# Kernel tuning notes

Hardware: AMD Instinct MI355X
Metric: run time of the kernel (lower is better)

Reference implementation:

```python
import jax, jax.numpy as jnp
import numpy as np

B, Z_DIM, T_DIM, ACT_E, CF, N_ACT, STEPS = 256, 256, 512, 256, 1024, 64, 64


def setup_inputs() -> dict:
    key = jax.random.key(0)
    ks = jax.random.split(key, 12)
    s = 0.02
    def n(k, shape):
        return jax.random.normal(k, shape, jnp.float32) * s
    return {
        "z": jax.random.normal(ks[0], (B, Z_DIM), jnp.float32),
        "W_z2t": n(ks[1], (T_DIM, Z_DIM)), "b_z2t": jnp.zeros((T_DIM,), jnp.float32),
        "E": n(ks[2], (N_ACT, ACT_E)),  # encoder_act2e embedding table
        "Wih_a": n(ks[3], (4 * CF, T_DIM + ACT_E)), "Whh_a": n(ks[4], (4 * CF, CF)),
        "bih_a": jnp.zeros((4 * CF,), jnp.float32), "bhh_a": jnp.zeros((4 * CF,), jnp.float32),
        "Wih_t": n(ks[5], (4 * CF, T_DIM + ACT_E + 1)), "Whh_t": n(ks[6], (4 * CF, CF)),
        "bih_t": jnp.zeros((4 * CF,), jnp.float32), "bhh_t": jnp.zeros((4 * CF,), jnp.float32),
        "W_act": n(ks[7], (N_ACT, CF)), "b_act": jnp.zeros((N_ACT,), jnp.float32),
        "W_ts1": n(ks[8], (CF // 2, CF)), "b_ts1": jnp.zeros((CF // 2,), jnp.float32),
        "W_ts2": n(ks[9], (1, CF // 2)), "b_ts2": jnp.zeros((1,), jnp.float32),
    }


def _lstm_step(x, h, c, Wih, Whh, bih, bhh):
    # PyTorch LSTM gate order: i, f, g, o
    gates = x @ Wih.T + h @ Whh.T + bih + bhh
    i, f, g, o = jnp.split(gates, 4, axis=-1)
    c = jax.nn.sigmoid(f) * c + jax.nn.sigmoid(i) * jnp.tanh(g)
    h = jax.nn.sigmoid(o) * jnp.tanh(c)
    return h, c


def reference(z, W_z2t, b_z2t, E, Wih_a, Whh_a, bih_a, bhh_a,
              Wih_t, Whh_t, bih_t, bhh_t, W_act, b_act,
              W_ts1, b_ts1, W_ts2, b_ts2):
    Bz = z.shape[0]
    t_rec = jax.nn.relu(z @ W_z2t.T + b_z2t)                 # [B, t_dim]
    zeros_h = jnp.zeros((Bz, CF), z.dtype)
    act_emb0 = jnp.broadcast_to(E[-1], (Bz, ACT_E))          # EOT token embedding
    ts0 = jnp.zeros((Bz, 1), z.dtype)

    def step(carry, _):
        h_a, c_a, h_t, c_t, act_emb, ts = carry
        x_a = jnp.concatenate([t_rec, act_emb], axis=1)       # [B, t_dim+act_e]
        h_a, c_a = _lstm_step(x_a, h_a, c_a, Wih_a, Whh_a, bih_a, bhh_a)
        logits = h_a @ W_act.T + b_act                        # [B, num_activities]
        act_emb = E[jnp.argmax(logits, axis=1)]               # [B, act_e]
        x_t = jnp.concatenate([t_rec, act_emb, ts], axis=1)   # [B, t_dim+act_e+1]
        h_t, c_t = _lstm_step(x_t, h_t, c_t, Wih_t, Whh_t, bih_t, bhh_t)
        ts = jax.nn.relu(h_t @ W_ts1.T + b_ts1) @ W_ts2.T + b_ts2  # [B, 1]
        return (h_a, c_a, h_t, c_t, act_emb, ts), (logits, ts)

    carry0 = (zeros_h, zeros_h, zeros_h, zeros_h, act_emb0, ts0)
    _, (logits_seq, ts_seq) = jax.lax.scan(step, carry0, None, length=STEPS)
    acts_rec = jax.nn.softmax(jnp.transpose(logits_seq, (1, 0, 2)), axis=2)  # [B, T, A]
    ts_rec = jnp.transpose(ts_seq[..., 0], (1, 0))                            # [B, T]
    return acts_rec, ts_rec
```

## Files before the change

kernel.cpp:

```cpp
#include <hip/hip_runtime.h>
#include <stdint.h>

typedef unsigned int u32;
typedef float  f32x4 __attribute__((ext_vector_type(4)));
typedef float  f32x2 __attribute__((ext_vector_type(2)));
typedef double f64x2 __attribute__((ext_vector_type(2)));
typedef double f64x4 __attribute__((ext_vector_type(4)));

constexpr int NT = 256;
constexpr int BB = 256;
constexpr int ZD = 256;
constexpr int TD = 512;
constexpr int CF = 1024;
constexpr int G4 = 4096;
constexpr int NA = 64;
constexpr int NSTEP = 64;
constexpr int TS_OFF = BB * NSTEP * NA;

constexpr int RSF = 34;
constexpr int FRS = 68;
constexpr int SMEMB = 2 * 64 * RSF * 8;

struct P {
  const float *z, *W_z2t, *b_z2t, *E, *Wih_a, *Whh_a, *bih_a, *bhh_a,
              *Wih_t, *Whh_t, *bih_t, *bhh_t, *W_act, *b_act, *W_ts1, *b_ts1, *W_ts2, *b_ts2;
  float* out;
  double *t_rec64, *pre_a64, *E_proj_a64, *h_a64, *c_a64, *gacc_a;
  float *t_rec32, *pre_t, *E_proj_t, *colt, *h_t, *c_t, *gacc_t, *ts_accum;
  int* idxb;
};

__device__ __forceinline__ float sigf(float x){ return 1.f / (1.f + expf(-x)); }
__device__ __forceinline__ float tanhf_(float x){
  float ax = fabsf(x); float e = expf(-2.f * ax);
  float t = 1.f - 2.f * e / (1.f + e);
  return x < 0.f ? -t : t;
}
__device__ __forceinline__ double sigd(double x){ return 1.0 / (1.0 + exp(-x)); }

__global__ void __launch_bounds__(NT) k_setup(P p){
  __shared__ double sz[ZD];
  const int bid = blockIdx.x, tid = threadIdx.x;
  for (int i = tid; i < ZD; i += NT) sz[i] = (double)p.z[bid * ZD + i];
  __syncthreads();
  for (int k = tid; k < TD; k += NT){
    const float* wr = p.W_z2t + (size_t)k * ZD;
    double a = 0.0;
    for (int j = 0; j < ZD; ++j) a = fma((double)wr[j], sz[j], a);
    a += (double)p.b_z2t[k];
    double t = a > 0.0 ? a : 0.0;
    p.t_rec64[(size_t)bid * TD + k] = t;
    p.t_rec32[(size_t)bid * TD + k] = (float)t;
  }
  for (int i = tid; i < CF; i += NT){
    p.c_a64[(size_t)bid * CF + i] = 0.0;
    p.h_a64[(size_t)bid * CF + i] = 0.0;
    p.c_t[(size_t)bid * CF + i] = 0.f;
    p.h_t[(size_t)bid * CF + i] = 0.f;
  }
  if (tid == 0){ p.idxb[bid] = NA - 1; p.ts_accum[bid] = 0.f; }
}

__global__ void __launch_bounds__(NT) k_eproj(P p){
  __shared__ double sz[ZD];
  const int bid = blockIdx.x, tid = threadIdx.x;
  if (bid < 256){
    const int erow = bid >> 2, cchunk = bid & 3;
    for (int i = tid; i < ZD; i += NT) sz[i] = (double)p.E[erow * ZD + i];
    __syncthreads();
    for (int ci = 0; ci < 4; ++ci){
      const int c = cchunk * 1024 + ci * 256 + tid;
      const float* wr = p.Wih_a + (size_t)c * 768 + 512;
      double a = 0.0;
      for (int j = 0; j < 256; ++j) a = fma((double)wr[j], sz[j], a);
      p.E_proj_a64[(size_t)erow * G4 + c] = a;
    }
  } else if (bid < 512){
    const int erow = (bid - 256) >> 2, cchunk = (bid - 256) & 3;
    for (int i = tid; i < ZD; i += NT) sz[i] = (double)p.E[erow * ZD + i];
    __syncthreads();
    for (int ci = 0; ci < 4; ++ci){
      const int c = cchunk * 1024 + ci * 256 + tid;
      const float* wr = p.Wih_t + (size_t)c * 769 + 512;
      float a = 0.f;
      for (int j = 0; j < 256; ++j) a = fmaf(wr[j], (float)sz[j], a);
      p.E_proj_t[(size_t)erow * G4 + c] = a;
    }
  } else {
    const int c = (bid - 512) * 256 + tid;
    p.colt[c] = p.Wih_t[(size_t)c * 769 + 768];
  }
}

template <bool A64, bool OUT64, bool BIAS>
__device__ void mgemm64(char* smem, const void* __restrict__ Av, int lda,
                        const float* __restrict__ B, int ldb,
                        int rowb, int colb, int K,
                        const void* __restrict__ addin,
                        const float* __restrict__ bih, const float* __restrict__ bhh,
                        void* __restrict__ outv){
  double* As = (double*)smem;
  double* Bs = As + 64 * RSF;
  const int tid = threadIdx.x;
  const int lane = tid & 63;
  const int wm = (tid >> 7) & 1, wn = (tid >> 6) & 1;
  const int m = lane & 15, q = lane >> 4;
  const int tr = tid >> 2, tkq = tid & 3;
  const double* A64p = (const double*)Av;
  const float*  A32p = (const float*)Av;

  double av[8], bv[8];
  auto loadchunk = [&](int kb){
    if (A64){
      const double* ap = A64p + (size_t)(rowb + tr) * lda + kb + tkq * 8;
      #pragma unroll
      for (int j = 0; j < 8; ++j) av[j] = ap[j];
    } else {
      const float* ap = A32p + (size_t)(rowb + tr) * lda + kb + tkq * 8;
      #pragma unroll
      for (int j = 0; j < 8; ++j) av[j] = (double)ap[j];
    }
    const float* bp = B + (size_t)(colb + tr) * ldb + kb + tkq * 8;
    #pragma unroll
    for (int j = 0; j < 8; ++j) bv[j] = (double)bp[j];
  };
  f64x4 acc[2][2];
  #pragma unroll
  for (int g = 0; g < 2; ++g)
    #pragma unroll
    for (int h = 0; h < 2; ++h) acc[g][h] = f64x4{0.0,0.0,0.0,0.0};

  loadchunk(0);
  for (int kb = 0; kb < K; kb += 32){
    __syncthreads();
    {
      double* arow = As + tr * RSF + tkq * 8;
      double* brow = Bs + tr * RSF + tkq * 8;
      #pragma unroll
      for (int j = 0; j < 4; ++j){
        *(f64x2*)(arow + j * 2) = f64x2{av[j], av[j + 4]};
        *(f64x2*)(brow + j * 2) = f64x2{bv[j], bv[j + 4]};
      }
    }
    __syncthreads();
    if (kb + 32 < K) loadchunk(kb + 32);
    #pragma unroll
    for (int sp = 0; sp < 4; ++sp){
      const f64x2 a0 = *(const f64x2*)(As + (wm * 32 +  0 + m) * RSF + sp * 8 + q * 2);
      const f64x2 a1 = *(const f64x2*)(As + (wm * 32 + 16 + m) * RSF + sp * 8 + q * 2);
      const f64x2 b0 = *(const f64x2*)(Bs + (wn * 32 +  0 + m) * RSF + sp * 8 + q * 2);
      const f64x2 b1 = *(const f64x2*)(Bs + (wn * 32 + 16 + m) * RSF + sp * 8 + q * 2);
      acc[0][0] = __builtin_amdgcn_mfma_f64_16x16x4f64(a0[0], b0[0], acc[0][0], 0, 0, 0);
      acc[0][1] = __builtin_amdgcn_mfma_f64_16x16x4f64(a0[0], b1[0], acc[0][1], 0, 0, 0);
      acc[1][0] = __builtin_amdgcn_mfma_f64_16x16x4f64(a1[0], b0[0], acc[1][0], 0, 0, 0);
      acc[1][1] = __builtin_amdgcn_mfma_f64_16x16x4f64(a1[0], b1[0], acc[1][1], 0, 0, 0);
      acc[0][0] = __builtin_amdgcn_mfma_f64_16x16x4f64(a0[1], b0[1], acc[0][0], 0, 0, 0);
      acc[0][1] = __builtin_amdgcn_mfma_f64_16x16x4f64(a0[1], b1[1], acc[0][1], 0, 0, 0);
      acc[1][0] = __builtin_amdgcn_mfma_f64_16x16x4f64(a1[1], b0[1], acc[1][0], 0, 0, 0);
      acc[1][1] = __builtin_amdgcn_mfma_f64_16x16x4f64(a1[1], b1[1], acc[1][1], 0, 0, 0);
    }
  }
  #pragma unroll
  for (int g = 0; g < 2; ++g){
    const int rb = rowb + wm * 32 + g * 16 + q;
    #pragma unroll
    for (int h = 0; h < 2; ++h){
      const int cc = colb + wn * 32 + h * 16 + m;
      if (BIAS){
        const double bb = (double)bih[cc] + (double)bhh[cc];
        #pragma unroll
        for (int v = 0; v < 4; ++v){
          if (OUT64) ((double*)outv)[(size_t)(rb + 4 * v) * G4 + cc] = acc[g][h][v] + bb;
          else       ((float*) outv)[(size_t)(rb + 4 * v) * G4 + cc] = (float)(acc[g][h][v] + bb);
        }
      } else {
        #pragma unroll
        for (int v = 0; v < 4; ++v){
          const size_t o = (size_t)(rb + 4 * v) * G4 + cc;
          if (OUT64) ((double*)outv)[o] = acc[g][h][v] + ((const double*)addin)[o];
          else       ((float*) outv)[o] = (float)(acc[g][h][v] + (double)((const float*)addin)[o]);
        }
      }
    }
  }
}

template <bool BIAS>
__device__ void dgemm32(char* smem, const float* __restrict__ A, int lda,
                        const float* __restrict__ B, int ldb,
                        int rowb, int colb, int K,
                        const float* __restrict__ addin,
                        const float* __restrict__ bih, const float* __restrict__ bhh,
                        float* __restrict__ outp){
  float* As = (float*)smem;
  float* Bs = (float*)(smem + 64 * FRS * 4);
  const int tid = threadIdx.x;
  const int tx = tid & 15, ty = tid >> 4;
  const int r_ = tid >> 2, kq = tid & 3;
  const int wsw = r_ ^ (kq * 8);
  float acc[4][4];
  #pragma unroll
  for (int i = 0; i < 4; ++i)
    #pragma unroll
    for (int j = 0; j < 4; ++j) acc[i][j] = 0.f;

  float pa[16], pb[16];
  auto ldA = [&](int kb){
    const float* ap = A + (size_t)(rowb + r_) * lda + kb + kq * 16;
    #pragma unroll
    for (int j = 0; j < 16; ++j) pa[j] = ap[j];
  };
  auto ldB = [&](int kb){
    const float* bp = B + (size_t)(colb + r_) * ldb + kb + kq * 16;
    #pragma unroll
    for (int j = 0; j < 16; ++j) pb[j] = bp[j];
  };
  ldA(0); ldB(0);
  for (int kb = 0; kb < K; kb += 64){
    __syncthreads();
    #pragma unroll
    for (int j = 0; j < 16; ++j){
      As[(kq * 16 + j) * FRS + wsw] = pa[j];
      Bs[(kq * 16 + j) * FRS + wsw] = pb[j];
    }
    __syncthreads();
    if (kb + 64 < K){ ldA(kb + 64); ldB(kb + 64); }
    #pragma unroll 4
    for (int k = 0; k < 64; ++k){
      const int sw = (k >> 4) * 8;
      f32x4 a4 = *(const f32x4*)(As + k * FRS + ((4 * ty) ^ sw));
      f32x4 b4 = *(const f32x4*)(Bs + k * FRS + ((4 * tx) ^ sw));
      acc[0][0] = fmaf(a4[0], b4[0], acc[0][0]); acc[0][1] = fmaf(a4[0], b4[1], acc[0][1]);
      acc[0][2] = fmaf(a4[0], b4[2], acc[0][2]); acc[0][3] = fmaf(a4[0], b4[3], acc[0][3]);
      acc[1][0] = fmaf(a4[1], b4[0], acc[1][0]); acc[1][1] = fmaf(a4[1], b4[1], acc[1][1]);
      acc[1][2] = fmaf(a4[1], b4[2], acc[1][2]); acc[1][3] = fmaf(a4[1], b4[3], acc[1][3]);
      acc[2][0] = fmaf(a4[2], b4[0], acc[2][0]); acc[2][1] = fmaf(a4[2], b4[1], acc[2][1]);
      acc[2][2] = fmaf(a4[2], b4[2], acc[2][2]); acc[2][3] = fmaf(a4[2], b4[3], acc[2][3]);
      acc[3][0] = fmaf(a4[3], b4[0], acc[3][0]); acc[3][1] = fmaf(a4[3], b4[1], acc[3][1]);
      acc[3][2] = fmaf(a4[3], b4[2], acc[3][2]); acc[3][3] = fmaf(a4[3], b4[3], acc[3][3]);
    }
  }
  const int c0 = colb + 4 * tx;
  if (BIAS){
    float bb0 = bih[c0+0] + bhh[c0+0], bb1 = bih[c0+1] + bhh[c0+1];
    float bb2 = bih[c0+2] + bhh[c0+2], bb3 = bih[c0+3] + bhh[c0+3];
    #pragma unroll
    for (int i = 0; i < 4; ++i){
      float* o = outp + (size_t)(rowb + 4 * ty + i) * G4 + c0;
      o[0] = acc[i][0] + bb0; o[1] = acc[i][1] + bb1;
      o[2] = acc[i][2] + bb2; o[3] = acc[i][3] + bb3;
    }
  } else {
    #pragma unroll
    for (int i = 0; i < 4; ++i){
      const size_t base = (size_t)(rowb + 4 * ty + i) * G4 + c0;
      const float* ai = addin + base;
      float* o = outp + base;
      o[0] = acc[i][0] + ai[0]; o[1] = acc[i][1] + ai[1];
      o[2] = acc[i][2] + ai[2]; o[3] = acc[i][3] + ai[3];
    }
  }
}

__device__ void tshead_j(const P& p, int bid, int hbuf){
  const int tid = threadIdx.x;
  const int tm = bid >> 6, tjq = bid & 63;
  const int rowb = tm * 32;
  const int rt = tid >> 3, j8 = tid & 7;
  const int j = tjq * 8 + j8;
  const float* __restrict__ hr = p.h_t + (size_t)hbuf * BB * CF + (size_t)(rowb + rt) * CF;
  const float* __restrict__ wr = p.W_ts1 + (size_t)j * CF;
  float a0=0,a1=0,a2=0,a3=0;
  for (int k = 0; k < CF; k += 16){
    f32x4 h0 = *(const f32x4*)(hr + k),     h1 = *(const f32x4*)(hr + k + 4);
    f32x4 h2 = *(const f32x4*)(hr + k + 8), h3 = *(const f32x4*)(hr + k + 12);
    f32x4 w0 = *(const f32x4*)(wr + k),     w1 = *(const f32x4*)(wr + k + 4);
    f32x4 w2 = *(const f32x4*)(wr + k + 8), w3 = *(const f32x4*)(wr + k + 12);
    a0 = fmaf(h0[0],w0[0], fmaf(h0[1],w0[1], fmaf(h0[2],w0[2], fmaf(h0[3],w0[3], a0))));
    a1 = fmaf(h1[0],w1[0], fmaf(h1[1],w1[1], fmaf(h1[2],w1[2], fmaf(h1[3],w1[3], a1))));
    a2 = fmaf(h2[0],w2[0], fmaf(h2[1],w2[1], fmaf(h2[2],w2[2], fmaf(h2[3],w2[3], a2))));
    a3 = fmaf(h3[0],w3[0], fmaf(h3[1],w3[1], fmaf(h3[2],w3[2], fmaf(h3[3],w3[3], a3))));
  }
  float v = ((a0 + a1) + (a2 + a3)) + p.b_ts1[j];
  v = (v > 0.f ? v : 0.f) * p.W_ts2[j];
  v += __shfl_xor(v, 1, 64);
  v += __shfl_xor(v, 2, 64);
  v += __shfl_xor(v, 4, 64);
  if (j8 == 0) atomicAdd(p.ts_accum + rowb + rt, v);
}

__global__ void __launch_bounds__(NT) k_pre(P p){
  __shared__ __align__(16) char smem[SMEMB];
  const int bid = blockIdx.x;
  const int hsel = bid >> 8, sub = bid & 255;
  const int rowb = (sub >> 6) * 64, colb = (sub & 63) * 64;
  if (hsel == 0)
    mgemm64<true, true, true>(smem, p.t_rec64, TD, p.Wih_a, 768, rowb, colb, TD,
                              nullptr, p.bih_a, p.bhh_a, p.pre_a64);
  else
    dgemm32<true>(smem, p.t_rec32, TD, p.Wih_t, 769, rowb, colb, TD,
                  nullptr, p.bih_t, p.bhh_t, p.pre_t);
}

__global__ void __launch_bounds__(NT) k_stepA(P p, int s){
  __shared__ __align__(16) char smem[SMEMB];
  const int bid = blockIdx.x;
  if (s > 0) tshead_j(p, bid, s & 1);
  const int hsel = bid >> 8, sub = bid & 255;
  const int rowb = (sub >> 6) * 64, colb = (sub & 63) * 64;
  const int rd = s & 1;
  if (hsel == 0)
    mgemm64<true, true, false>(smem, p.h_a64 + (size_t)rd * BB * CF, CF, p.Whh_a, CF,
                               rowb, colb, CF, p.pre_a64, nullptr, nullptr, p.gacc_a);
  else
    dgemm32<false>(smem, p.h_t + (size_t)rd * BB * CF, CF, p.Whh_t, CF,
                   rowb, colb, CF, p.pre_t, nullptr, nullptr, p.gacc_t);
}

__global__ void __launch_bounds__(NT) k_stepB(P p, int s){
  __shared__ double shd[1092];
  const int b = blockIdx.x, tid = threadIdx.x;
  const int cur = (s + 1) & 1;
  int idxp = p.idxb[b];
  idxp = idxp < 0 ? 0 : (idxp > 63 ? 63 : idxp);
  {
    const double* ga = p.gacc_a + (size_t)b * G4;
    const double* ea = p.E_proj_a64 + (size_t)idxp * G4;
    const int c0 = tid * 4;
    #pragma unroll
    for (int jj = 0; jj < 4; ++jj){
      const int c = c0 + jj;
      double gi = ga[0*CF + c] + ea[0*CF + c];
      double gf = ga[1*CF + c] + ea[1*CF + c];
      double gg = ga[2*CF + c] + ea[2*CF + c];
      double go = ga[3*CF + c] + ea[3*CF + c];
      double cv = p.c_a64[(size_t)b * CF + c];
      double cn = sigd(gf) * cv + sigd(gi) * tanh(gg);
      double hn = sigd(go) * tanh(cn);
      p.c_a64[(size_t)b * CF + c] = cn;
      p.h_a64[(size_t)cur * BB * CF + (size_t)b * CF + c] = hn;
      shd[c] = hn;
    }
  }
  if (tid == 0) shd[1088] = (s == 0) ? 0.0 : ((double)p.ts_accum[b] + (double)p.b_ts2[0]);
  __syncthreads();
  {
    const int w = tid >> 6, l = tid & 63, l15 = l & 15, quad = l >> 4;
    const int a = w * 16 + l15;
    const float* wr = p.W_act + (size_t)a * CF + quad * 256;
    const double* hp = shd + quad * 256;
    double acc = 0.0;
    for (int kk = 0; kk < 256; kk += 4){
      acc = fma((double)wr[kk+0], hp[kk+0], acc);
      acc = fma((double)wr[kk+1], hp[kk+1], acc);
      acc = fma((double)wr[kk+2], hp[kk+2], acc);
      acc = fma((double)wr[kk+3], hp[kk+3], acc);
    }
    acc += __shfl_xor(acc, 16, 64);
    acc += __shfl_xor(acc, 32, 64);
    if (quad == 0) shd[1024 + a] = acc;
  }
  __syncthreads();
  if (tid < 64){
    double acc = shd[1024 + tid] + (double)p.b_act[tid];
    double m = acc;
    #pragma unroll
    for (int off = 32; off; off >>= 1) m = fmax(m, __shfl_xor(m, off, 64));
    unsigned long long ball = __ballot(acc == m);
    int idxv = __ffsll(ball) - 1;
    idxv = idxv < 0 ? 0 : (idxv > 63 ? 63 : idxv);
    double e = exp(acc - m);
    double ssum = e;
    #pragma unroll
    for (int off = 32; off; off >>= 1) ssum += __shfl_xor(ssum, off, 64);
    p.out[(size_t)b * (NSTEP * NA) + s * NA + tid] = (float)(e / ssum);
    if (tid == 0){
      p.idxb[b] = idxv;
      shd[1089] = (double)idxv;
      if (s > 0) p.out[TS_OFF + b * NSTEP + (s - 1)] = (float)shd[1088];
    }
  }
  __syncthreads();
  const float ts_val = (float)shd[1088];
  const int idxv = (int)shd[1089];
  const int c0 = tid * 4;
  const float* gb = p.gacc_t   + (size_t)b * G4;
  const float* eb = p.E_proj_t + (size_t)idxv * G4;
  f32x4 gi = *(const f32x4*)(gb + 0*CF + c0) + *(const f32x4*)(eb + 0*CF + c0) + ts_val * *(const f32x4*)(p.colt + 0*CF + c0);
  f32x4 gf = *(const f32x4*)(gb + 1*CF + c0) + *(const f32x4*)(eb + 1*CF + c0) + ts_val * *(const f32x4*)(p.colt + 1*CF + c0);
  f32x4 gg = *(const f32x4*)(gb + 2*CF + c0) + *(const f32x4*)(eb + 2*CF + c0) + ts_val * *(const f32x4*)(p.colt + 2*CF + c0);
  f32x4 go = *(const f32x4*)(gb + 3*CF + c0) + *(const f32x4*)(eb + 3*CF + c0) + ts_val * *(const f32x4*)(p.colt + 3*CF + c0);
  f32x4 cv = *(f32x4*)(p.c_t + (size_t)b * CF + c0);
  f32x4 cn, hn;
  #pragma unroll
  for (int jj = 0; jj < 4; ++jj){
    float cj = sigf(gf[jj]) * cv[jj] + sigf(gi[jj]) * tanhf_(gg[jj]);
    float hj = sigf(go[jj]) * tanhf_(cj);
    cn[jj] = cj; hn[jj] = hj;
  }
  *(f32x4*)(p.c_t + (size_t)b * CF + c0) = cn;
  *(f32x4*)(p.h_t + (size_t)cur * BB * CF + (size_t)b * CF + c0) = hn;
  __syncthreads();
  if (tid == 0) p.ts_accum[b] = 0.f;
}

__global__ void __launch_bounds__(NT) k_tsfin(P p){
  tshead_j(p, blockIdx.x, 0);
}
__global__ void __launch_bounds__(NT) k_tswrite(P p){
  p.out[TS_OFF + threadIdx.x * NSTEP + 63] = p.ts_accum[threadIdx.x] + p.b_ts2[0];
}

extern "C" void kernel_launch(void* const* d_in, const int* in_sizes, int n_in,
                              void* d_out, int out_size, void* d_ws, size_t ws_size,
                              hipStream_t stream){
  (void)in_sizes; (void)n_in; (void)out_size; (void)ws_size;
  P p;
  p.z     = (const float*)d_in[0];  p.W_z2t = (const float*)d_in[1];  p.b_z2t = (const float*)d_in[2];
  p.E     = (const float*)d_in[3];  p.Wih_a = (const float*)d_in[4];  p.Whh_a = (const float*)d_in[5];
  p.bih_a = (const float*)d_in[6];  p.bhh_a = (const float*)d_in[7];  p.Wih_t = (const float*)d_in[8];
  p.Whh_t = (const float*)d_in[9];  p.bih_t = (const float*)d_in[10]; p.bhh_t = (const float*)d_in[11];
  p.W_act = (const float*)d_in[12]; p.b_act = (const float*)d_in[13]; p.W_ts1 = (const float*)d_in[14];
  p.b_ts1 = (const float*)d_in[15]; p.W_ts2 = (const float*)d_in[16]; p.b_ts2 = (const float*)d_in[17];
  p.out = (float*)d_out;
  char* w = (char*)d_ws;
  size_t off = 0;
  auto alloc = [&](size_t bytes) -> void* { void* r = w + off; off += (bytes + 255) & ~(size_t)255; return r; };
  p.t_rec64    = (double*)alloc((size_t)BB * TD * 8);
  p.pre_a64    = (double*)alloc((size_t)BB * G4 * 8);
  p.E_proj_a64 = (double*)alloc((size_t)NA * G4 * 8);
  p.h_a64      = (double*)alloc((size_t)2 * BB * CF * 8);
  p.c_a64      = (double*)alloc((size_t)BB * CF * 8);
  p.gacc_a     = (double*)alloc((size_t)BB * G4 * 8);
  p.t_rec32    = (float*)alloc((size_t)BB * TD * 4);
  p.pre_t      = (float*)alloc((size_t)BB * G4 * 4);
  p.E_proj_t   = (float*)alloc((size_t)NA * G4 * 4);
  p.colt       = (float*)alloc((size_t)G4 * 4);
  p.h_t        = (float*)alloc((size_t)2 * BB * CF * 4);
  p.c_t        = (float*)alloc((size_t)BB * CF * 4);
  p.gacc_t     = (float*)alloc((size_t)BB * G4 * 4);
  p.ts_accum   = (float*)alloc((size_t)BB * 4);
  p.idxb       = (int*)  alloc((size_t)BB * 4);

  k_setup<<<dim3(256), dim3(NT), 0, stream>>>(p);
  k_eproj<<<dim3(528), dim3(NT), 0, stream>>>(p);
  k_pre  <<<dim3(512), dim3(NT), 0, stream>>>(p);
  for (int s = 0; s < NSTEP; ++s){
    k_stepA<<<dim3(512), dim3(NT), 0, stream>>>(p, s);
    k_stepB<<<dim3(256), dim3(NT), 0, stream>>>(p, s);
  }
  k_tsfin  <<<dim3(512), dim3(NT), 0, stream>>>(p);
  k_tswrite<<<dim3(1),   dim3(NT), 0, stream>>>(p);
}
```

Measured before the change: 11.42 ms.

## Replace LDS-staged recurrent GEMMs with direct global-load register-pipelined GEMMs

The per-step recurrent GEMMs (h_a@Whh_a in fp64 MFMA and h_t@Whh_t in fp32 FMA) now load operands straight from global memory into registers with a two-stage software prefetch, instead of staging tiles through shared memory with __syncthreads. The goal is to remove LDS traffic, barriers and shared-memory occupancy limits from the step kernel. The trade-off is that the new loads are strided and uncoalesced per lane and operands are fetched redundantly across threads, so the kernel depends on L1/L2 cache hits. The prologue GEMM keeps the old LDS path, now specialized to bias-only.

```diff
diff --git a/kernel.cpp b/kernel.cpp
--- a/kernel.cpp
+++ b/kernel.cpp
@@ -20,6 +20,7 @@
 constexpr int RSF = 34;
 constexpr int FRS = 68;
 constexpr int SMEMB = 2 * 64 * RSF * 8;
+
 
 struct P {
   const float *z, *W_z2t, *b_z2t, *E, *Wih_a, *Whh_a, *bih_a, *bhh_a,
@@ -92,11 +93,10 @@
   }
 }
 
-template <bool A64, bool OUT64, bool BIAS>
+template <bool A64, bool OUT64>
 __device__ void mgemm64(char* smem, const void* __restrict__ Av, int lda,
                         const float* __restrict__ B, int ldb,
                         int rowb, int colb, int K,
-                        const void* __restrict__ addin,
                         const float* __restrict__ bih, const float* __restrict__ bhh,
                         void* __restrict__ outv){
   double* As = (double*)smem;
@@ -166,30 +166,19 @@
     #pragma unroll
     for (int h = 0; h < 2; ++h){
       const int cc = colb + wn * 32 + h * 16 + m;
-      if (BIAS){
-        const double bb = (double)bih[cc] + (double)bhh[cc];
-        #pragma unroll
-        for (int v = 0; v < 4; ++v){
-          if (OUT64) ((double*)outv)[(size_t)(rb + 4 * v) * G4 + cc] = acc[g][h][v] + bb;
-          else       ((float*) outv)[(size_t)(rb + 4 * v) * G4 + cc] = (float)(acc[g][h][v] + bb);
-        }
-      } else {
-        #pragma unroll
-        for (int v = 0; v < 4; ++v){
-          const size_t o = (size_t)(rb + 4 * v) * G4 + cc;
-          if (OUT64) ((double*)outv)[o] = acc[g][h][v] + ((const double*)addin)[o];
-          else       ((float*) outv)[o] = (float)(acc[g][h][v] + (double)((const float*)addin)[o]);
-        }
+      const double bb = (double)bih[cc] + (double)bhh[cc];
+      #pragma unroll
+      for (int v = 0; v < 4; ++v){
+        if (OUT64) ((double*)outv)[(size_t)(rb + 4 * v) * G4 + cc] = acc[g][h][v] + bb;
+        else       ((float*) outv)[(size_t)(rb + 4 * v) * G4 + cc] = (float)(acc[g][h][v] + bb);
       }
     }
   }
 }
 
-template <bool BIAS>
 __device__ void dgemm32(char* smem, const float* __restrict__ A, int lda,
                         const float* __restrict__ B, int ldb,
                         int rowb, int colb, int K,
-                        const float* __restrict__ addin,
                         const float* __restrict__ bih, const float* __restrict__ bhh,
                         float* __restrict__ outp){
   float* As = (float*)smem;
@@ -241,24 +230,129 @@
     }
   }
   const int c0 = colb + 4 * tx;
-  if (BIAS){
-    float bb0 = bih[c0+0] + bhh[c0+0], bb1 = bih[c0+1] + bhh[c0+1];
-    float bb2 = bih[c0+2] + bhh[c0+2], bb3 = bih[c0+3] + bhh[c0+3];
-    #pragma unroll
-    for (int i = 0; i < 4; ++i){
-      float* o = outp + (size_t)(rowb + 4 * ty + i) * G4 + c0;
-      o[0] = acc[i][0] + bb0; o[1] = acc[i][1] + bb1;
-      o[2] = acc[i][2] + bb2; o[3] = acc[i][3] + bb3;
-    }
-  } else {
-    #pragma unroll
-    for (int i = 0; i < 4; ++i){
-      const size_t base = (size_t)(rowb + 4 * ty + i) * G4 + c0;
-      const float* ai = addin + base;
-      float* o = outp + base;
-      o[0] = acc[i][0] + ai[0]; o[1] = acc[i][1] + ai[1];
-      o[2] = acc[i][2] + ai[2]; o[3] = acc[i][3] + ai[3];
-    }
+  float bb0 = bih[c0+0] + bhh[c0+0], bb1 = bih[c0+1] + bhh[c0+1];
+  float bb2 = bih[c0+2] + bhh[c0+2], bb3 = bih[c0+3] + bhh[c0+3];
+  #pragma unroll
+  for (int i = 0; i < 4; ++i){
+    float* o = outp + (size_t)(rowb + 4 * ty + i) * G4 + c0;
+    o[0] = acc[i][0] + bb0; o[1] = acc[i][1] + bb1;
+    o[2] = acc[i][2] + bb2; o[3] = acc[i][3] + bb3;
+  }
+}
+
+template <bool A64, bool OUT64>
+__device__ void mgemm64d(const void* __restrict__ Av, int lda,
+                         const float* __restrict__ B, int ldb,
+                         int rowb, int colb, int K,
+                         const void* __restrict__ addin, void* __restrict__ outv){
+  const int tid = threadIdx.x, lane = tid & 63;
+  const int wm = (tid >> 7) & 1, wn = (tid >> 6) & 1;
+  const int m = lane & 15, q = lane >> 4;
+  const double* Ar0 = (const double*)Av + (size_t)(rowb + wm * 32 +  0 + m) * lda;
+  const double* Ar1 = (const double*)Av + (size_t)(rowb + wm * 32 + 16 + m) * lda;
+  const float*  Af0 = (const float*) Av + (size_t)(rowb + wm * 32 +  0 + m) * lda;
+  const float*  Af1 = (const float*) Av + (size_t)(rowb + wm * 32 + 16 + m) * lda;
+  const float*  Bc0 = B + (size_t)(colb + wn * 32 +  0 + m) * ldb;
+  const float*  Bc1 = B + (size_t)(colb + wn * 32 + 16 + m) * ldb;
+  f64x4 c00{0,0,0,0}, c01{0,0,0,0}, c10{0,0,0,0}, c11{0,0,0,0};
+  double xA00,xA04,xA10,xA14,xB00,xB04,xB10,xB14;
+  double yA00,yA04,yA10,yA14,yB00,yB04,yB10,yB14;
+#define ALD(S, g) do{ const int _k = 8 * (g) + q;                                 \
+    S##A00 = A64 ? Ar0[_k]     : (double)Af0[_k];                                 \
+    S##A04 = A64 ? Ar0[_k + 4] : (double)Af0[_k + 4];                             \
+    S##A10 = A64 ? Ar1[_k]     : (double)Af1[_k];                                 \
+    S##A14 = A64 ? Ar1[_k + 4] : (double)Af1[_k + 4];                             \
+    S##B00 = (double)Bc0[_k];   S##B04 = (double)Bc0[_k + 4];                     \
+    S##B10 = (double)Bc1[_k];   S##B14 = (double)Bc1[_k + 4]; }while(0)
+#define AMF(S) do{                                                                \
+    c00 = __builtin_amdgcn_mfma_f64_16x16x4f64(S##A00, S##B00, c00, 0, 0, 0);     \
+    c01 = __builtin_amdgcn_mfma_f64_16x16x4f64(S##A00, S##B10, c01, 0, 0, 0);     \
+    c10 = __builtin_amdgcn_mfma_f64_16x16x4f64(S##A10, S##B00, c10, 0, 0, 0);     \
+    c11 = __builtin_amdgcn_mfma_f64_16x16x4f64(S##A10, S##B10, c11, 0, 0, 0);     \
+    c00 = __builtin_amdgcn_mfma_f64_16x16x4f64(S##A04, S##B04, c00, 0, 0, 0);     \
+    c01 = __builtin_amdgcn_mfma_f64_16x16x4f64(S##A04, S##B14, c01, 0, 0, 0);     \
+    c10 = __builtin_amdgcn_mfma_f64_16x16x4f64(S##A14, S##B04, c10, 0, 0, 0);     \
+    c11 = __builtin_amdgcn_mfma_f64_16x16x4f64(S##A14, S##B14, c11, 0, 0, 0); }while(0)
+  const int NG = K >> 3;
+  ALD(x, 0);
+  for (int g = 0; g < NG; g += 2){
+    ALD(y, g + 1);
+    AMF(x);
+    if (g + 2 < NG) ALD(x, g + 2);
+    AMF(y);
+  }
+#undef ALD
+#undef AMF
+  #pragma unroll
+  for (int g = 0; g < 2; ++g){
+    const int rb = rowb + wm * 32 + g * 16 + q;
+    #pragma unroll
+    for (int h = 0; h < 2; ++h){
+      const f64x4 a = g ? (h ? c11 : c10) : (h ? c01 : c00);
+      const int cc = colb + wn * 32 + h * 16 + m;
+      #pragma unroll
+      for (int v = 0; v < 4; ++v){
+        const size_t o = (size_t)(rb + 4 * v) * G4 + cc;
+        if (OUT64) ((double*)outv)[o] = a[v] + ((const double*)addin)[o];
+        else       ((float*) outv)[o] = (float)(a[v] + (double)((const float*)addin)[o]);
+      }
+    }
+  }
+}
+
+__device__ void dgemm32d(const float* __restrict__ A, int lda,
+                         const float* __restrict__ B, int ldb,
+                         int rowb, int colb, int K,
+                         const float* __restrict__ addin, float* __restrict__ outp){
+  const int tid = threadIdx.x;
+  const int tx = tid & 15, ty = tid >> 4;
+  const float* ar0 = A + (size_t)(rowb + 4 * ty + 0) * lda;
+  const float* ar1 = A + (size_t)(rowb + 4 * ty + 1) * lda;
+  const float* ar2 = A + (size_t)(rowb + 4 * ty + 2) * lda;
+  const float* ar3 = A + (size_t)(rowb + 4 * ty + 3) * lda;
+  const float* br0 = B + (size_t)(colb + 4 * tx + 0) * ldb;
+  const float* br1 = B + (size_t)(colb + 4 * tx + 1) * ldb;
+  const float* br2 = B + (size_t)(colb + 4 * tx + 2) * ldb;
+  const float* br3 = B + (size_t)(colb + 4 * tx + 3) * ldb;
+  float acc[4][4];
+  #pragma unroll
+  for (int i = 0; i < 4; ++i)
+    #pragma unroll
+    for (int j = 0; j < 4; ++j) acc[i][j] = 0.f;
+  f32x4 xa0,xa1,xa2,xa3, xb0,xb1,xb2,xb3;
+  f32x4 ya0,ya1,ya2,ya3, yb0,yb1,yb2,yb3;
+#define TLD(S, kk) do{                                                            \
+    S##a0 = *(const f32x4*)(ar0 + (kk)); S##a1 = *(const f32x4*)(ar1 + (kk));     \
+    S##a2 = *(const f32x4*)(ar2 + (kk)); S##a3 = *(const f32x4*)(ar3 + (kk));     \
+    S##b0 = *(const f32x4*)(br0 + (kk)); S##b1 = *(const f32x4*)(br1 + (kk));     \
+    S##b2 = *(const f32x4*)(br2 + (kk)); S##b3 = *(const f32x4*)(br3 + (kk)); }while(0)
+#define TFMA(S) do{ _Pragma("unroll")                                             \
+    for (int _kk = 0; _kk < 4; ++_kk){                                            \
+      acc[0][0]=fmaf(S##a0[_kk],S##b0[_kk],acc[0][0]); acc[0][1]=fmaf(S##a0[_kk],S##b1[_kk],acc[0][1]); \
+      acc[0][2]=fmaf(S##a0[_kk],S##b2[_kk],acc[0][2]); acc[0][3]=fmaf(S##a0[_kk],S##b3[_kk],acc[0][3]); \
+      acc[1][0]=fmaf(S##a1[_kk],S##b0[_kk],acc[1][0]); acc[1][1]=fmaf(S##a1[_kk],S##b1[_kk],acc[1][1]); \
+      acc[1][2]=fmaf(S##a1[_kk],S##b2[_kk],acc[1][2]); acc[1][3]=fmaf(S##a1[_kk],S##b3[_kk],acc[1][3]); \
+      acc[2][0]=fmaf(S##a2[_kk],S##b0[_kk],acc[2][0]); acc[2][1]=fmaf(S##a2[_kk],S##b1[_kk],acc[2][1]); \
+      acc[2][2]=fmaf(S##a2[_kk],S##b2[_kk],acc[2][2]); acc[2][3]=fmaf(S##a2[_kk],S##b3[_kk],acc[2][3]); \
+      acc[3][0]=fmaf(S##a3[_kk],S##b0[_kk],acc[3][0]); acc[3][1]=fmaf(S##a3[_kk],S##b1[_kk],acc[3][1]); \
+      acc[3][2]=fmaf(S##a3[_kk],S##b2[_kk],acc[3][2]); acc[3][3]=fmaf(S##a3[_kk],S##b3[_kk],acc[3][3]); } }while(0)
+  TLD(x, 0);
+  for (int kb = 0; kb < K; kb += 8){
+    TLD(y, kb + 4);
+    TFMA(x);
+    if (kb + 8 < K) TLD(x, kb + 8);
+    TFMA(y);
+  }
+#undef TLD
+#undef TFMA
+  const int c0 = colb + 4 * tx;
+  #pragma unroll
+  for (int i = 0; i < 4; ++i){
+    const size_t base = (size_t)(rowb + 4 * ty + i) * G4 + c0;
+    const float* ai = addin + base;
+    float* o = outp + base;
+    o[0] = acc[i][0] + ai[0]; o[1] = acc[i][1] + ai[1];
+    o[2] = acc[i][2] + ai[2]; o[3] = acc[i][3] + ai[3];
   }
 }
 
@@ -295,26 +389,25 @@
   const int hsel = bid >> 8, sub = bid & 255;
   const int rowb = (sub >> 6) * 64, colb = (sub & 63) * 64;
   if (hsel == 0)
-    mgemm64<true, true, true>(smem, p.t_rec64, TD, p.Wih_a, 768, rowb, colb, TD,
-                              nullptr, p.bih_a, p.bhh_a, p.pre_a64);
+    mgemm64<true, true>(smem, p.t_rec64, TD, p.Wih_a, 768, rowb, colb, TD,
+                        p.bih_a, p.bhh_a, p.pre_a64);
   else
-    dgemm32<true>(smem, p.t_rec32, TD, p.Wih_t, 769, rowb, colb, TD,
-                  nullptr, p.bih_t, p.bhh_t, p.pre_t);
+    dgemm32(smem, p.t_rec32, TD, p.Wih_t, 769, rowb, colb, TD,
+            p.bih_t, p.bhh_t, p.pre_t);
 }
 
 __global__ void __launch_bounds__(NT) k_stepA(P p, int s){
-  __shared__ __align__(16) char smem[SMEMB];
   const int bid = blockIdx.x;
   if (s > 0) tshead_j(p, bid, s & 1);
   const int hsel = bid >> 8, sub = bid & 255;
   const int rowb = (sub >> 6) * 64, colb = (sub & 63) * 64;
   const int rd = s & 1;
   if (hsel == 0)
-    mgemm64<true, true, false>(smem, p.h_a64 + (size_t)rd * BB * CF, CF, p.Whh_a, CF,
-                               rowb, colb, CF, p.pre_a64, nullptr, nullptr, p.gacc_a);
+    mgemm64d<true, true>(p.h_a64 + (size_t)rd * BB * CF, CF, p.Whh_a, CF,
+                         rowb, colb, CF, p.pre_a64, p.gacc_a);
   else
-    dgemm32<false>(smem, p.h_t + (size_t)rd * BB * CF, CF, p.Whh_t, CF,
-                   rowb, colb, CF, p.pre_t, nullptr, nullptr, p.gacc_t);
+    dgemm32d(p.h_t + (size_t)rd * BB * CF, CF, p.Whh_t, CF,
+             rowb, colb, CF, p.pre_t, p.gacc_t);
 }
 
 __global__ void __launch_bounds__(NT) k_stepB(P p, int s){
```

Result: slower. 22.06 ms (+93.1%).

## Split recurrent step GEMMs into smaller 32x32 tiles with 128-thread blocks

Applied to the files above, without the earlier changes.

The per-step recurrent GEMMs move from 64x64 tiles on 256-thread blocks to 32x32 tiles on 128-thread blocks, so each step launches 2048 blocks instead of 512. The fp64 path now keeps the B operand in LDS as fp32 and converts it to fp64 at the MFMA. The ts-head work is redistributed over the first 1024 blocks. This is meant to fill more of the CUs during the latency-bound serial steps, at the cost of less operand reuse per block and more global traffic.

```diff
diff --git a/kernel.cpp b/kernel.cpp
--- a/kernel.cpp
+++ b/kernel.cpp
@@ -7,7 +7,8 @@
 typedef double f64x2 __attribute__((ext_vector_type(2)));
 typedef double f64x4 __attribute__((ext_vector_type(4)));
 
-constexpr int NT = 256;
+constexpr int NT  = 256;
+constexpr int NTA = 128;
 constexpr int BB = 256;
 constexpr int ZD = 256;
 constexpr int TD = 512;
@@ -20,6 +21,13 @@
 constexpr int RSF = 34;
 constexpr int FRS = 68;
 constexpr int SMEMB = 2 * 64 * RSF * 8;
+
+constexpr int ARS_A = 34;
+constexpr int ASZ_A = 32 * ARS_A * 8;
+constexpr int BSZ_A = 32 * ARS_A * 4;
+constexpr int TRS   = 36;
+constexpr int TSZ   = 32 * TRS * 4;
+constexpr int SMEMA = (ASZ_A + BSZ_A) > (2 * TSZ) ? (ASZ_A + BSZ_A) : (2 * TSZ);
 
 struct P {
   const float *z, *W_z2t, *b_z2t, *E, *Wih_a, *Whh_a, *bih_a, *bhh_a,
@@ -92,13 +100,12 @@
   }
 }
 
-template <bool A64, bool OUT64, bool BIAS>
-__device__ void mgemm64(char* smem, const void* __restrict__ Av, int lda,
-                        const float* __restrict__ B, int ldb,
-                        int rowb, int colb, int K,
-                        const void* __restrict__ addin,
-                        const float* __restrict__ bih, const float* __restrict__ bhh,
-                        void* __restrict__ outv){
+template <bool A64, bool OUT64>
+__device__ void mgemm64s(char* smem, const void* __restrict__ Av, int lda,
+                         const float* __restrict__ B, int ldb,
+                         int rowb, int colb, int K,
+                         const float* __restrict__ bih, const float* __restrict__ bhh,
+                         void* __restrict__ outv){
   double* As = (double*)smem;
   double* Bs = As + 64 * RSF;
   const int tid = threadIdx.x;
@@ -166,32 +173,21 @@
     #pragma unroll
     for (int h = 0; h < 2; ++h){
       const int cc = colb + wn * 32 + h * 16 + m;
-      if (BIAS){
-        const double bb = (double)bih[cc] + (double)bhh[cc];
-        #pragma unroll
-        for (int v = 0; v < 4; ++v){
-          if (OUT64) ((double*)outv)[(size_t)(rb + 4 * v) * G4 + cc] = acc[g][h][v] + bb;
-          else       ((float*) outv)[(size_t)(rb + 4 * v) * G4 + cc] = (float)(acc[g][h][v] + bb);
-        }
-      } else {
-        #pragma unroll
-        for (int v = 0; v < 4; ++v){
-          const size_t o = (size_t)(rb + 4 * v) * G4 + cc;
-          if (OUT64) ((double*)outv)[o] = acc[g][h][v] + ((const double*)addin)[o];
-          else       ((float*) outv)[o] = (float)(acc[g][h][v] + (double)((const float*)addin)[o]);
-        }
+      const double bb = (double)bih[cc] + (double)bhh[cc];
+      #pragma unroll
+      for (int v = 0; v < 4; ++v){
+        if (OUT64) ((double*)outv)[(size_t)(rb + 4 * v) * G4 + cc] = acc[g][h][v] + bb;
+        else       ((float*) outv)[(size_t)(rb + 4 * v) * G4 + cc] = (float)(acc[g][h][v] + bb);
       }
     }
   }
 }
 
-template <bool BIAS>
-__device__ void dgemm32(char* smem, const float* __restrict__ A, int lda,
-                        const float* __restrict__ B, int ldb,
-                        int rowb, int colb, int K,
-                        const float* __restrict__ addin,
-                        const float* __restrict__ bih, const float* __restrict__ bhh,
-                        float* __restrict__ outp){
+__device__ void dgemm32s(char* smem, const float* __restrict__ A, int lda,
+                         const float* __restrict__ B, int ldb,
+                         int rowb, int colb, int K,
+                         const float* __restrict__ bih, const float* __restrict__ bhh,
+                         float* __restrict__ outp){
   float* As = (float*)smem;
   float* Bs = (float*)(smem + 64 * FRS * 4);
   const int tid = threadIdx.x;
@@ -241,24 +237,127 @@
     }
   }
   const int c0 = colb + 4 * tx;
-  if (BIAS){
-    float bb0 = bih[c0+0] + bhh[c0+0], bb1 = bih[c0+1] + bhh[c0+1];
-    float bb2 = bih[c0+2] + bhh[c0+2], bb3 = bih[c0+3] + bhh[c0+3];
-    #pragma unroll
-    for (int i = 0; i < 4; ++i){
-      float* o = outp + (size_t)(rowb + 4 * ty + i) * G4 + c0;
-      o[0] = acc[i][0] + bb0; o[1] = acc[i][1] + bb1;
-      o[2] = acc[i][2] + bb2; o[3] = acc[i][3] + bb3;
-    }
-  } else {
-    #pragma unroll
-    for (int i = 0; i < 4; ++i){
-      const size_t base = (size_t)(rowb + 4 * ty + i) * G4 + c0;
-      const float* ai = addin + base;
-      float* o = outp + base;
-      o[0] = acc[i][0] + ai[0]; o[1] = acc[i][1] + ai[1];
-      o[2] = acc[i][2] + ai[2]; o[3] = acc[i][3] + ai[3];
-    }
+  float bb0 = bih[c0+0] + bhh[c0+0], bb1 = bih[c0+1] + bhh[c0+1];
+  float bb2 = bih[c0+2] + bhh[c0+2], bb3 = bih[c0+3] + bhh[c0+3];
+  #pragma unroll
+  for (int i = 0; i < 4; ++i){
+    float* o = outp + (size_t)(rowb + 4 * ty + i) * G4 + c0;
+    o[0] = acc[i][0] + bb0; o[1] = acc[i][1] + bb1;
+    o[2] = acc[i][2] + bb2; o[3] = acc[i][3] + bb3;
+  }
+}
+
+__device__ void mgemm64w(char* smem, const double* __restrict__ A, int lda,
+                         const float* __restrict__ B, int ldb,
+                         int rowb, int colb, int K,
+                         const double* __restrict__ addin, double* __restrict__ outp){
+  double* As = (double*)smem;
+  float*  Bs = (float*)(smem + ASZ_A);
+  const int tid = threadIdx.x, lane = tid & 63;
+  const int w = tid >> 6;
+  const int m = lane & 15, q = lane >> 4;
+  const int tr = tid >> 2, tkq = tid & 3;
+  double av[8]; float bv[8];
+  auto loadchunk = [&](int kb){
+    const double* ap = A + (size_t)(rowb + tr) * lda + kb + tkq * 8;
+    #pragma unroll
+    for (int j = 0; j < 8; ++j) av[j] = ap[j];
+    const float* bp = B + (size_t)(colb + tr) * ldb + kb + tkq * 8;
+    #pragma unroll
+    for (int j = 0; j < 8; ++j) bv[j] = bp[j];
+  };
+  f64x4 acc0{0,0,0,0}, acc1{0,0,0,0};
+  loadchunk(0);
+  for (int kb = 0; kb < K; kb += 32){
+    __syncthreads();
+    {
+      double* arow = As + tr * ARS_A + tkq * 8;
+      float*  brow = Bs + tr * ARS_A + tkq * 8;
+      #pragma unroll
+      for (int j = 0; j < 4; ++j){
+        *(f64x2*)(arow + j * 2) = f64x2{av[j], av[j + 4]};
+        *(f32x2*)(brow + j * 2) = f32x2{bv[j], bv[j + 4]};
+      }
+    }
+    __syncthreads();
+    if (kb + 32 < K) loadchunk(kb + 32);
+    #pragma unroll
+    for (int sp = 0; sp < 4; ++sp){
+      const f64x2 a0  = *(const f64x2*)(As + (16 * w + m) * ARS_A + sp * 8 + q * 2);
+      const f32x2 b0f = *(const f32x2*)(Bs + ( 0 + m) * ARS_A + sp * 8 + q * 2);
+      const f32x2 b1f = *(const f32x2*)(Bs + (16 + m) * ARS_A + sp * 8 + q * 2);
+      acc0 = __builtin_amdgcn_mfma_f64_16x16x4f64(a0[0], (double)b0f[0], acc0, 0, 0, 0);
+      acc1 = __builtin_amdgcn_mfma_f64_16x16x4f64(a0[0], (double)b1f[0], acc1, 0, 0, 0);
+      acc0 = __builtin_amdgcn_mfma_f64_16x16x4f64(a0[1], (double)b0f[1], acc0, 0, 0, 0);
+      acc1 = __builtin_amdgcn_mfma_f64_16x16x4f64(a0[1], (double)b1f[1], acc1, 0, 0, 0);
+    }
+  }
+  const int rb = rowb + 16 * w + q;
+  #pragma unroll
+  for (int h = 0; h < 2; ++h){
+    const f64x4 a = h ? acc1 : acc0;
+    const int cc = colb + h * 16 + m;
+    #pragma unroll
+    for (int v = 0; v < 4; ++v){
+      const size_t o = (size_t)(rb + 4 * v) * G4 + cc;
+      outp[o] = a[v] + addin[o];
+    }
+  }
+}
+
+__device__ void dgemm32w(char* smem, const float* __restrict__ A, int lda,
+                         const float* __restrict__ B, int ldb,
+                         int rowb, int colb, int K,
+                         const float* __restrict__ addin, float* __restrict__ outp){
+  float* As = (float*)smem;
+  float* Bs = (float*)(smem + TSZ);
+  const int tid = threadIdx.x;
+  const int tx = tid & 7, ty = tid >> 3;
+  const int r_ = tid >> 2, kq = tid & 3;
+  const int wsw = r_ ^ (kq * 8);
+  float acc[2][4];
+  #pragma unroll
+  for (int i = 0; i < 2; ++i)
+    #pragma unroll
+    for (int j = 0; j < 4; ++j) acc[i][j] = 0.f;
+  float pa[8], pb[8];
+  auto ldAB = [&](int kb){
+    const float* ap = A + (size_t)(rowb + r_) * lda + kb + kq * 8;
+    #pragma unroll
+    for (int j = 0; j < 8; ++j) pa[j] = ap[j];
+    const float* bp = B + (size_t)(colb + r_) * ldb + kb + kq * 8;
+    #pragma unroll
+    for (int j = 0; j < 8; ++j) pb[j] = bp[j];
+  };
+  ldAB(0);
+  for (int kb = 0; kb < K; kb += 32){
+    __syncthreads();
+    #pragma unroll
+    for (int j = 0; j < 8; ++j){
+      As[(kq * 8 + j) * TRS + wsw] = pa[j];
+      Bs[(kq * 8 + j) * TRS + wsw] = pb[j];
+    }
+    __syncthreads();
+    if (kb + 32 < K) ldAB(kb + 32);
+    #pragma unroll 4
+    for (int k = 0; k < 32; ++k){
+      const int sw = (k >> 3) * 8;
+      f32x2 a2 = *(const f32x2*)(As + k * TRS + ((2 * ty) ^ sw));
+      f32x4 b4 = *(const f32x4*)(Bs + k * TRS + ((4 * tx) ^ sw));
+      acc[0][0] = fmaf(a2[0], b4[0], acc[0][0]); acc[0][1] = fmaf(a2[0], b4[1], acc[0][1]);
+      acc[0][2] = fmaf(a2[0], b4[2], acc[0][2]); acc[0][3] = fmaf(a2[0], b4[3], acc[0][3]);
+      acc[1][0] = fmaf(a2[1], b4[0], acc[1][0]); acc[1][1] = fmaf(a2[1], b4[1], acc[1][1]);
+      acc[1][2] = fmaf(a2[1], b4[2], acc[1][2]); acc[1][3] = fmaf(a2[1], b4[3], acc[1][3]);
+    }
+  }
+  const int c0 = colb + 4 * tx;
+  #pragma unroll
+  for (int i = 0; i < 2; ++i){
+    const size_t base = (size_t)(rowb + 2 * ty + i) * G4 + c0;
+    const float* ai = addin + base;
+    float* o = outp + base;
+    o[0] = acc[i][0] + ai[0]; o[1] = acc[i][1] + ai[1];
+    o[2] = acc[i][2] + ai[2]; o[3] = acc[i][3] + ai[3];
   }
 }
 
@@ -289,32 +388,58 @@
   if (j8 == 0) atomicAdd(p.ts_accum + rowb + rt, v);
 }
 
+__device__ void tshead_j128(const P& p, int bid, int hbuf){
+  const int tid = threadIdx.x;
+  const int tm = bid >> 7, tjq = bid & 127;
+  const int rowb = tm * 32;
+  const int rt = tid >> 2, j4 = tid & 3;
+  const int j = tjq * 4 + j4;
+  const float* __restrict__ hr = p.h_t + (size_t)hbuf * BB * CF + (size_t)(rowb + rt) * CF;
+  const float* __restrict__ wr = p.W_ts1 + (size_t)j * CF;
+  float a0=0,a1=0,a2=0,a3=0;
+  for (int k = 0; k < CF; k += 16){
+    f32x4 h0 = *(const f32x4*)(hr + k),     h1 = *(const f32x4*)(hr + k + 4);
+    f32x4 h2 = *(const f32x4*)(hr + k + 8), h3 = *(const f32x4*)(hr + k + 12);
+    f32x4 w0 = *(const f32x4*)(wr + k),     w1 = *(const f32x4*)(wr + k + 4);
+    f32x4 w2 = *(const f32x4*)(wr + k + 8), w3 = *(const f32x4*)(wr + k + 12);
+    a0 = fmaf(h0[0],w0[0], fmaf(h0[1],w0[1], fmaf(h0[2],w0[2], fmaf(h0[3],w0[3], a0))));
+    a1 = fmaf(h1[0],w1[0], fmaf(h1[1],w1[1], fmaf(h1[2],w1[2], fmaf(h1[3],w1[3], a1))));
+    a2 = fmaf(h2[0],w2[0], fmaf(h2[1],w2[1], fmaf(h2[2],w2[2], fmaf(h2[3],w2[3], a2))));
+    a3 = fmaf(h3[0],w3[0], fmaf(h3[1],w3[1], fmaf(h3[2],w3[2], fmaf(h3[3],w3[3], a3))));
+  }
+  float v = ((a0 + a1) + (a2 + a3)) + p.b_ts1[j];
+  v = (v > 0.f ? v : 0.f) * p.W_ts2[j];
+  v += __shfl_xor(v, 1, 64);
+  v += __shfl_xor(v, 2, 64);
+  if (j4 == 0) atomicAdd(p.ts_accum + rowb + rt, v);
+}
+
 __global__ void __launch_bounds__(NT) k_pre(P p){
   __shared__ __align__(16) char smem[SMEMB];
   const int bid = blockIdx.x;
   const int hsel = bid >> 8, sub = bid & 255;
   const int rowb = (sub >> 6) * 64, colb = (sub & 63) * 64;
   if (hsel == 0)
-    mgemm64<true, true, true>(smem, p.t_rec64, TD, p.Wih_a, 768, rowb, colb, TD,
-                              nullptr, p.bih_a, p.bhh_a, p.pre_a64);
+    mgemm64s<true, true>(smem, p.t_rec64, TD, p.Wih_a, 768, rowb, colb, TD,
+                         p.bih_a, p.bhh_a, p.pre_a64);
   else
-    dgemm32<true>(smem, p.t_rec32, TD, p.Wih_t, 769, rowb, colb, TD,
-                  nullptr, p.bih_t, p.bhh_t, p.pre_t);
-}
-
-__global__ void __launch_bounds__(NT) k_stepA(P p, int s){
-  __shared__ __align__(16) char smem[SMEMB];
+    dgemm32s(smem, p.t_rec32, TD, p.Wih_t, 769, rowb, colb, TD,
+             p.bih_t, p.bhh_t, p.pre_t);
+}
+
+__global__ void __launch_bounds__(NTA) k_stepA(P p, int s){
+  __shared__ __align__(16) char smem[SMEMA];
   const int bid = blockIdx.x;
-  if (s > 0) tshead_j(p, bid, s & 1);
-  const int hsel = bid >> 8, sub = bid & 255;
-  const int rowb = (sub >> 6) * 64, colb = (sub & 63) * 64;
+  if (s > 0 && bid < 1024) tshead_j128(p, bid, s & 1);
+  const int hsel = bid >> 10, sub = bid & 1023;
+  const int rowb = (sub >> 7) * 32, colb = (sub & 127) * 32;
   const int rd = s & 1;
   if (hsel == 0)
-    mgemm64<true, true, false>(smem, p.h_a64 + (size_t)rd * BB * CF, CF, p.Whh_a, CF,
-                               rowb, colb, CF, p.pre_a64, nullptr, nullptr, p.gacc_a);
+    mgemm64w(smem, p.h_a64 + (size_t)rd * BB * CF, CF, p.Whh_a, CF,
+             rowb, colb, CF, p.pre_a64, p.gacc_a);
   else
-    dgemm32<false>(smem, p.h_t + (size_t)rd * BB * CF, CF, p.Whh_t, CF,
-                   rowb, colb, CF, p.pre_t, nullptr, nullptr, p.gacc_t);
+    dgemm32w(smem, p.h_t + (size_t)rd * BB * CF, CF, p.Whh_t, CF,
+             rowb, colb, CF, p.pre_t, p.gacc_t);
 }
 
 __global__ void __launch_bounds__(NT) k_stepB(P p, int s){
@@ -446,8 +571,8 @@
   k_eproj<<<dim3(528), dim3(NT), 0, stream>>>(p);
   k_pre  <<<dim3(512), dim3(NT), 0, stream>>>(p);
   for (int s = 0; s < NSTEP; ++s){
-    k_stepA<<<dim3(512), dim3(NT), 0, stream>>>(p, s);
-    k_stepB<<<dim3(256), dim3(NT), 0, stream>>>(p, s);
+    k_stepA<<<dim3(2048), dim3(NTA), 0, stream>>>(p, s);
+    k_stepB<<<dim3(256),  dim3(NT),  0, stream>>>(p, s);
   }
   k_tsfin  <<<dim3(512), dim3(NT), 0, stream>>>(p);
   k_tswrite<<<dim3(1),   dim3(NT), 0, stream>>>(p);
```

Result: faster. 10.10 ms (-11.5%).
